# Performance work log

Measured on AMD Instinct MI355X. Metric: run time of the kernel, lower is better.

Reference implementation:

```python
import jax, jax.numpy as jnp
import numpy as np

S, B, DENC, DD, DE, V, T = 49, 64, 512, 1800, 512, 10000, 20


def setup_inputs() -> dict:
    key = jax.random.key(0)
    ks = jax.random.split(key, 16)
    g = lambda i, shape: jax.random.normal(ks[i], shape, jnp.float32) * 0.02
    z = lambda *shape: jnp.zeros(shape, jnp.float32)
    return {
        "h": jax.random.normal(ks[0], (S, B, DENC), jnp.float32),
        "E": jax.random.randint(ks[1], (T, B), 0, V),
        "emb": g(2, (V, DE)),
        "attn_W1": g(3, (DD, DD + DENC)), "attn_b1": z(DD),
        "attn_w2": g(4, (DD,)), "attn_b2": z(),
        "beta_w": g(5, (DD,)), "beta_b": z(),
        "W_ih": g(6, (4 * DD, DE + DENC)), "W_hh": g(7, (4 * DD, DD)),
        "b_ih": z(4 * DD), "b_hh": z(4 * DD),
        "out_W": g(8, (V, DD + DE + DENC)), "out_b": z(V),
        "ih_W1": g(9, (DD, DENC)), "ih_b1": z(DD), "ih_W2": g(10, (DD, DD)), "ih_b2": z(DD),
        "ic_W1": g(11, (DD, DENC)), "ic_b1": z(DD), "ic_W2": g(12, (DD, DD)), "ic_b2": z(DD),
    }


def _mlp(x, W1, b1, W2, b2):
    return jax.nn.relu(x @ W1.T + b1) @ W2.T + b2


def reference(h, E, emb, attn_W1, attn_b1, attn_w2, attn_b2, beta_w, beta_b,
              W_ih, W_hh, b_ih, b_hh, out_W, out_b,
              ih_W1, ih_b1, ih_W2, ih_b2, ic_W1, ic_b1, ic_W2, ic_b2):
    # h: (S, B, DENC) encoder annotations; E: (T, B) teacher tokens.
    h_avg = h.mean(axis=0)                        # (B, DENC)
    h0 = _mlp(h_avg, ih_W1, ih_b1, ih_W2, ih_b2)  # (B, DD)
    c0 = _mlp(h_avg, ic_W1, ic_b1, ic_W2, ic_b2)  # (B, DD)
    tok0 = jnp.zeros((h.shape[1],), jnp.int32)    # first y_tm1 is token 0

    def step(carry, e_t):
        ht, ct, prev_tok = carry
        # --- additive attention (queries=ht, keys=values=h) ---
        qexp = jnp.broadcast_to(ht[None], h.shape[:2] + (ht.shape[-1],))  # (S,B,DD)
        zpre = jnp.concatenate([qexp, h], axis=-1)                        # (S,B,DD+DENC)
        u = jax.nn.relu(zpre @ attn_W1.T + attn_b1) @ attn_w2 + attn_b2   # (S,B)
        a = jax.nn.softmax(u, axis=0)                                     # softmax over seq
        ctx = jnp.einsum('sb,sbe->be', a, h)                              # (B,DENC)
        beta = jax.nn.sigmoid(ht @ beta_w + beta_b)                       # (B,)
        ctx = ctx * beta[:, None]
        # --- LSTM cell on [embed(E_tm1); context] ---
        x = jnp.concatenate([emb[e_t], ctx], axis=-1)                     # (B,DE+DENC)
        gates = x @ W_ih.T + b_ih + ht @ W_hh.T + b_hh                    # (B,4*DD)
        i_g, f_g, g_g, o_g = jnp.split(gates, 4, axis=-1)
        c_new = jax.nn.sigmoid(f_g) * ct + jax.nn.sigmoid(i_g) * jnp.tanh(g_g)
        h_new = jax.nn.sigmoid(o_g) * jnp.tanh(c_new)
        # --- deep output layer: [h_t; embed(argmax prev logits); ctx] ---
        y_emb = emb[prev_tok]
        logits = jnp.concatenate([h_new, y_emb, ctx], axis=-1) @ out_W.T + out_b
        return (h_new, c_new, jnp.argmax(logits, axis=-1).astype(jnp.int32)), logits

    _, logits = jax.lax.scan(step, (h0, c0, tok0), E[:-1])
    return logits  # (T-1, B, V)
```

## Files before the change

### kernel.cpp

```cpp
#include <hip/hip_runtime.h>
#include <hip/hip_bf16.h>
#include <cmath>


namespace {

constexpr int S = 49, B = 64, DENC = 512, DD = 1800, DE = 512, V = 10000, T = 20;
constexpr int KC = DD + DE + DENC;
constexpr int G4 = 4 * DD;
constexpr int KCP = 2848;
constexpr int DDP = 1824;

typedef __attribute__((ext_vector_type(8))) short short8;
typedef __attribute__((ext_vector_type(4))) float f32x4;

__device__ inline float sigf(float x) { return 1.f / (1.f + expf(-x)); }

__device__ inline ushort f2bf_rne(float x) {
  unsigned u = __float_as_uint(x);
  unsigned r = (u + 0x7FFFu + ((u >> 16) & 1u)) >> 16;
  return (ushort)r;
}
__device__ inline void split1(float x, ushort& h, ushort& l) {
  h = f2bf_rne(x);
  float hf = __uint_as_float(((unsigned)h) << 16);
  l = f2bf_rne(x - hf);
}
__device__ inline void split8(float4 a, float4 b, short8& hi, short8& lo) {
  float v[8] = {a.x, a.y, a.z, a.w, b.x, b.y, b.z, b.w};
#pragma unroll
  for (int i = 0; i < 8; ++i) {
    ushort h, l; split1(v[i], h, l);
    hi[i] = (short)h; lo[i] = (short)l;
  }
}
__device__ inline unsigned fkey(float f) {
  unsigned u = __float_as_uint(f);
  return (u & 0x80000000u) ? ~u : (u | 0x80000000u);
}

__global__ __launch_bounds__(256) void hmean_kernel(const float* __restrict__ h,
                                                    float* __restrict__ h_avg) {
  int idx = blockIdx.x * 256 + threadIdx.x;
  if (idx >= B * DENC) return;
  float s = 0.f;
  for (int si = 0; si < S; ++si) s += h[(size_t)si * B * DENC + idx];
  h_avg[idx] = s * (1.0f / (float)S);
}

__global__ __launch_bounds__(256) void mfma_gemm9(
    const ushort* __restrict__ Ahi, const ushort* __restrict__ Alo, int ldap,
    const float* __restrict__ Wa, int ldwa, int Ka,
    const float* __restrict__ Wb, int ldwb, int K,
    float* __restrict__ P, int M, int N, int KP, int kchunk) {
  __shared__ float lds[2][6144];
  const int tid = threadIdx.x;
  const int lane = tid & 63;
  const int wv = tid >> 6;
  const int bn = blockIdx.x * 128;
  const int bm = blockIdx.y * 64;
  const int z = blockIdx.z;
  const int row = lane & 15;
  const int k_begin = z * kchunk;
  const int k_end = min(KP, k_begin + kchunk);

  auto stage = [&](int buf, int k0) {
#pragma unroll
    for (int q = 0; q < 4; ++q) {
      const int u = (wv * 4 + q) * 64 + lane;
      const int lr = u >> 3;
      const int pb = u & 7;
      int col = k0 + (pb ^ (lr & 7)) * 4;
      if (col >= K) col = 0;
      int grow = bn + lr;
      if (grow >= N) grow = N - 1;
      const float* src = (col < Ka) ? (Wa + (size_t)grow * ldwa + col)
                                    : (Wb + (size_t)grow * ldwb + (col - Ka));
      __builtin_amdgcn_global_load_lds(
          (const __attribute__((address_space(1))) unsigned int*)src,
          (__attribute__((address_space(3))) unsigned int*)
              &lds[buf][(wv * 4 + q) * 256 + lane * 4],
          16, 0, 0);
    }
    {
      const int u = wv * 64 + lane;
      const int lr = u >> 2;
      const int pb = u & 3;
      const int col = k0 + (pb ^ (lr & 3)) * 8;
      const ushort* sH = Ahi + (size_t)(bm + lr) * ldap + col;
      const ushort* sL = Alo + (size_t)(bm + lr) * ldap + col;
      __builtin_amdgcn_global_load_lds(
          (const __attribute__((address_space(1))) unsigned int*)sH,
          (__attribute__((address_space(3))) unsigned int*)
              &lds[buf][4096 + u * 4], 16, 0, 0);
      __builtin_amdgcn_global_load_lds(
          (const __attribute__((address_space(1))) unsigned int*)sL,
          (__attribute__((address_space(3))) unsigned int*)
              &lds[buf][5120 + u * 4], 16, 0, 0);
    }
  };

  f32x4 acc[2][4] = {};
  const int nsteps = (k_end > k_begin) ? ((k_end - k_begin) >> 5) : 0;
  if (nsteps) stage(0, k_begin);
  __syncthreads();

  for (int t = 0; t < nsteps; ++t) {
    const int cur = t & 1;
    if (t + 1 < nsteps) stage(cur ^ 1, k_begin + (t + 1) * 32);
    const int c0 = (lane >> 4) * 2;
    float4 w0a, w1a, w0b, w1b;
    {
      const int lrw = wv * 32 + row;
      const float* wb = &lds[cur][lrw * 32];
      w0a = *(const float4*)(wb + ((c0 ^ (lrw & 7)) * 4));
      w1a = *(const float4*)(wb + (((c0 + 1) ^ (lrw & 7)) * 4));
    }
    {
      const int lrw = wv * 32 + 16 + row;
      const float* wb = &lds[cur][lrw * 32];
      w0b = *(const float4*)(wb + ((c0 ^ (lrw & 7)) * 4));
      w1b = *(const float4*)(wb + (((c0 + 1) ^ (lrw & 7)) * 4));
    }
    short8 ah[4], al[4];
#pragma unroll
    for (int ms = 0; ms < 4; ++ms) {
      const int lra = ms * 16 + row;
      const int ca = lane >> 4;
      const int pc = (ca ^ (lra & 3)) * 4;
      ah[ms] = *(const short8*)(&lds[cur][4096 + lra * 16] + pc);
      al[ms] = *(const short8*)(&lds[cur][5120 + lra * 16] + pc);
    }
    short8 wh0, wl0, wh1, wl1;
    split8(w0a, w1a, wh0, wl0);
    split8(w0b, w1b, wh1, wl1);
#pragma unroll
    for (int ms = 0; ms < 4; ++ms) {
      acc[0][ms] = __builtin_amdgcn_mfma_f32_16x16x32_bf16(ah[ms], wh0, acc[0][ms], 0, 0, 0);
      acc[0][ms] = __builtin_amdgcn_mfma_f32_16x16x32_bf16(al[ms], wh0, acc[0][ms], 0, 0, 0);
      acc[0][ms] = __builtin_amdgcn_mfma_f32_16x16x32_bf16(ah[ms], wl0, acc[0][ms], 0, 0, 0);
      acc[1][ms] = __builtin_amdgcn_mfma_f32_16x16x32_bf16(ah[ms], wh1, acc[1][ms], 0, 0, 0);
      acc[1][ms] = __builtin_amdgcn_mfma_f32_16x16x32_bf16(al[ms], wh1, acc[1][ms], 0, 0, 0);
      acc[1][ms] = __builtin_amdgcn_mfma_f32_16x16x32_bf16(ah[ms], wl1, acc[1][ms], 0, 0, 0);
    }
    __syncthreads();
  }

  float* Pz = P + (size_t)z * ((size_t)M * N);
#pragma unroll
  for (int j = 0; j < 2; ++j) {
    const int n = bn + wv * 32 + j * 16 + row;
    if (n >= N) continue;
#pragma unroll
    for (int ms = 0; ms < 4; ++ms) {
      int r0 = bm + ms * 16 + (lane >> 4) * 4;
#pragma unroll
      for (int r = 0; r < 4; ++r)
        Pz[(size_t)(r0 + r) * N + n] = acc[j][ms][r];
    }
  }
}

template <int ACT>
__global__ __launch_bounds__(256) void reduce_k(const float* __restrict__ P, int nz,
                                                int total4, size_t MN, int N,
                                                const float* __restrict__ bias,
                                                float* __restrict__ C) {
  int i4 = blockIdx.x * 256 + threadIdx.x;
  if (i4 >= total4) return;
  size_t idx = (size_t)i4 * 4;
  float4 s = *(const float4*)(P + idx);
  for (int zz = 1; zz < nz; ++zz) {
    float4 t = *(const float4*)(P + (size_t)zz * MN + idx);
    s.x += t.x; s.y += t.y; s.z += t.z; s.w += t.w;
  }
  if (bias) {
    int nn = (int)(idx % (size_t)N);
    s.x += bias[nn]; s.y += bias[nn + 1]; s.z += bias[nn + 2]; s.w += bias[nn + 3];
  }
  if (ACT == 1) {
    s.x = fmaxf(s.x, 0.f); s.y = fmaxf(s.y, 0.f);
    s.z = fmaxf(s.z, 0.f); s.w = fmaxf(s.w, 0.f);
  }
  *(float4*)(C + idx) = s;
}

__global__ __launch_bounds__(256) void reduce_lg(const float* __restrict__ P, int nz,
                                                 const float* __restrict__ bias,
                                                 float* __restrict__ C,
                                                 unsigned long long* __restrict__ amax) {
  const int seg = blockIdx.x, b = blockIdx.y;
  const int tid = threadIdx.x;
  const size_t MN = (size_t)B * V;
  unsigned long long best = 0;
  for (int i = tid; i < 250; i += 256) {
    const int n = seg * 1000 + i * 4;
    const size_t idx = (size_t)b * V + n;
    float4 s = *(const float4*)(P + idx);
    for (int zz = 1; zz < nz; ++zz) {
      float4 t = *(const float4*)(P + (size_t)zz * MN + idx);
      s.x += t.x; s.y += t.y; s.z += t.z; s.w += t.w;
    }
    s.x += bias[n]; s.y += bias[n + 1]; s.z += bias[n + 2]; s.w += bias[n + 3];
    *(float4*)(C + idx) = s;
    float v[4] = {s.x, s.y, s.z, s.w};
#pragma unroll
    for (int j = 0; j < 4; ++j) {
      unsigned long long k =
          ((unsigned long long)fkey(v[j]) << 32) | (unsigned)(~(n + j));
      if (k > best) best = k;
    }
  }
  for (int off = 32; off; off >>= 1) {
    unsigned long long o = __shfl_xor(best, off);
    if (o > best) best = o;
  }
  __shared__ unsigned long long red[4];
  if ((tid & 63) == 0) red[tid >> 6] = best;
  __syncthreads();
  if (tid == 0) {
    for (int w = 1; w < 4; ++w)
      if (red[w] > best) best = red[w];
    atomicMax(&amax[b], best);
  }
}

__global__ __launch_bounds__(256) void split_row(
    const float* __restrict__ Wa, int ldwa, int Ka,
    int KP, ushort* __restrict__ hi, ushort* __restrict__ lo) {
  const int r = blockIdx.x;
  const float* ra = Wa + (size_t)r * ldwa;
  ushort* hr = hi + (size_t)r * KP;
  ushort* lr = lo + (size_t)r * KP;
  for (int k = threadIdx.x * 4; k < KP; k += 1024) {
    float4 v = {0.f, 0.f, 0.f, 0.f};
    if (k + 4 <= Ka) v = *(const float4*)(ra + k);
    ushort h0, l0, h1, l1, h2, l2, h3, l3;
    split1(v.x, h0, l0); split1(v.y, h1, l1);
    split1(v.z, h2, l2); split1(v.w, h3, l3);
    ushort4 hv = {h0, h1, h2, h3}, lv = {l0, l1, l2, l3};
    *(ushort4*)(hr + k) = hv;
    *(ushort4*)(lr + k) = lv;
  }
}

__global__ __launch_bounds__(256) void attn_u_kernel(const float* __restrict__ Q,
                                                     const float* __restrict__ Hproj,
                                                     const float* __restrict__ w2,
                                                     const float* __restrict__ b2,
                                                     float* __restrict__ u) {
  int s = blockIdx.x, b = blockIdx.y;
  const float4* q4 = (const float4*)(Q + (size_t)b * DD);
  const float4* h4 = (const float4*)(Hproj + ((size_t)s * B + b) * DD);
  const float4* w4 = (const float4*)w2;
  float acc = 0.f;
  for (int i = threadIdx.x; i < DD / 4; i += 256) {
    float4 q = q4[i], hh = h4[i], w = w4[i];
    acc += fmaxf(q.x + hh.x, 0.f) * w.x + fmaxf(q.y + hh.y, 0.f) * w.y +
           fmaxf(q.z + hh.z, 0.f) * w.z + fmaxf(q.w + hh.w, 0.f) * w.w;
  }
  for (int off = 32; off; off >>= 1) acc += __shfl_xor(acc, off);
  __shared__ float red[4];
  if ((threadIdx.x & 63) == 0) red[threadIdx.x >> 6] = acc;
  __syncthreads();
  if (threadIdx.x == 0) u[s * B + b] = red[0] + red[1] + red[2] + red[3] + b2[0];
}

__global__ __launch_bounds__(256) void softmax_ctx_pack(
    const float* __restrict__ u, const float* __restrict__ h,
    const float* __restrict__ ht, const float* __restrict__ beta_w,
    const float* __restrict__ beta_b, const float* __restrict__ emb,
    const int* __restrict__ Et, const unsigned long long* __restrict__ amax,
    ushort* __restrict__ xcat_hi, ushort* __restrict__ xcat_lo,
    ushort* __restrict__ cat2_hi, ushort* __restrict__ cat2_lo) {
  int b = blockIdx.x, slice = blockIdx.y, tid = threadIdx.x;
  __shared__ float a_sh[S];
  __shared__ float red[4];
  float uv = (tid < S) ? u[tid * B + b] : -INFINITY;
  float m = uv;
  for (int off = 32; off; off >>= 1) m = fmaxf(m, __shfl_xor(m, off));
  if ((tid & 63) == 0) red[tid >> 6] = m;
  __syncthreads();
  m = fmaxf(fmaxf(red[0], red[1]), fmaxf(red[2], red[3]));
  float e = (tid < S) ? expf(uv - m) : 0.f;
  float ssum = e;
  for (int off = 32; off; off >>= 1) ssum += __shfl_xor(ssum, off);
  __syncthreads();
  if ((tid & 63) == 0) red[tid >> 6] = ssum;
  __syncthreads();
  ssum = red[0] + red[1] + red[2] + red[3];
  if (tid < S) a_sh[tid] = e / ssum;
  float acc = 0.f;
  {
    const float4* h4 = (const float4*)(ht + (size_t)b * DD);
    const float4* w4 = (const float4*)beta_w;
    for (int i = tid; i < DD / 4; i += 256) {
      float4 x = h4[i], w = w4[i];
      acc += x.x * w.x + x.y * w.y + x.z * w.z + x.w * w.w;
    }
  }
  for (int off = 32; off; off >>= 1) acc += __shfl_xor(acc, off);
  __syncthreads();
  if ((tid & 63) == 0) red[tid >> 6] = acc;
  __syncthreads();
  float beta = sigf(red[0] + red[1] + red[2] + red[3] + beta_b[0]);

  const size_t xb = (size_t)b * KCP;
  for (int e0 = slice * 128 + tid; e0 < slice * 128 + 128; e0 += 256) {
    float c = 0.f;
    for (int si = 0; si < S; ++si) c += a_sh[si] * h[((size_t)si * B + b) * DENC + e0];
    c *= beta;
    ushort hh, ll; split1(c, hh, ll);
    xcat_hi[xb + DE + e0] = hh;      xcat_lo[xb + DE + e0] = ll;
    cat2_hi[xb + DD + DE + e0] = hh; cat2_lo[xb + DD + DE + e0] = ll;
  }
  int et = Et[b];
  int pt = (int)(~(unsigned)(amax[b] & 0xFFFFFFFFull));
  for (int e0 = slice * 128 + tid; e0 < slice * 128 + 128; e0 += 256) {
    ushort hh, ll;
    split1(emb[(size_t)et * DE + e0], hh, ll);
    xcat_hi[xb + e0] = hh; xcat_lo[xb + e0] = ll;
    split1(emb[(size_t)pt * DE + e0], hh, ll);
    cat2_hi[xb + DD + e0] = hh; cat2_lo[xb + DD + e0] = ll;
  }
  for (int j = slice * 450 + tid; j < slice * 450 + 450; j += 256) {
    ushort hh, ll; split1(ht[(size_t)b * DD + j], hh, ll);
    xcat_hi[xb + DE + DENC + j] = hh; xcat_lo[xb + DE + DENC + j] = ll;
  }
  if (slice == 3 && tid < KCP - KC) {
    xcat_hi[xb + KC + tid] = 0; xcat_lo[xb + KC + tid] = 0;
    cat2_hi[xb + KC + tid] = 0; cat2_lo[xb + KC + tid] = 0;
  }
}

__global__ __launch_bounds__(256) void lstm_fused(
    const float* __restrict__ P, int nz, const float* __restrict__ b_ih,
    const float* __restrict__ b_hh, float* __restrict__ ct, float* __restrict__ ht,
    ushort* __restrict__ cat2_hi, ushort* __restrict__ cat2_lo,
    ushort* __restrict__ ht_hi, ushort* __restrict__ ht_lo,
    unsigned long long* __restrict__ amax) {
  int idx = blockIdx.x * 256 + threadIdx.x;
  if (idx < B) amax[idx] = 0ull;
  if (idx >= B * DD) return;
  int b = idx / DD, d = idx % DD;
  const size_t MN = (size_t)B * G4;
  float g0 = 0.f, g1 = 0.f, g2 = 0.f, g3 = 0.f;
  for (int zz = 0; zz < nz; ++zz) {
    const float* g = P + (size_t)zz * MN + (size_t)b * G4;
    g0 += g[d]; g1 += g[DD + d]; g2 += g[2 * DD + d]; g3 += g[3 * DD + d];
  }
  g0 += b_ih[d] + b_hh[d];
  g1 += b_ih[DD + d] + b_hh[DD + d];
  g2 += b_ih[2 * DD + d] + b_hh[2 * DD + d];
  g3 += b_ih[3 * DD + d] + b_hh[3 * DD + d];
  float c = sigf(g1) * ct[idx] + sigf(g0) * tanhf(g2);
  float hn = sigf(g3) * tanhf(c);
  ct[idx] = c;
  ht[idx] = hn;
  ushort hh, ll; split1(hn, hh, ll);
  cat2_hi[(size_t)b * KCP + d] = hh; cat2_lo[(size_t)b * KCP + d] = ll;
  ht_hi[(size_t)b * DDP + d] = hh;   ht_lo[(size_t)b * DDP + d] = ll;
  if (d < DDP - DD) {
    ht_hi[(size_t)b * DDP + DD + d] = 0; ht_lo[(size_t)b * DDP + DD + d] = 0;
  }
}

__global__ void init_amax(unsigned long long* amax) {
  if (threadIdx.x < B) amax[threadIdx.x] = 0x00000000FFFFFFFFull;
}

constexpr size_t OFF_HAVG  = 0;
constexpr size_t OFF_TMP   = OFF_HAVG + 32768;
constexpr size_t OFF_HT    = OFF_TMP + 115200;
constexpr size_t OFF_CT    = OFF_HT + 115200;
constexpr size_t OFF_HPROJ = OFF_CT + 115200;
constexpr size_t OFF_Q     = OFF_HPROJ + 5644800;
constexpr size_t OFF_U     = OFF_Q + 115200;
constexpr size_t OFF_TOK   = OFF_U + 3200;
constexpr size_t OFF_PBUF  = OFF_TOK + 128;
constexpr size_t PBUF_F    = 6400000;
constexpr size_t OFF_USH   = OFF_PBUF + PBUF_F;

constexpr size_t U_HT_HI  = 0;
constexpr size_t U_HT_LO  = U_HT_HI + (size_t)B * DDP;
constexpr size_t U_XC_HI  = U_HT_LO + (size_t)B * DDP;
constexpr size_t U_XC_LO  = U_XC_HI + (size_t)B * KCP;
constexpr size_t U_C2_HI  = U_XC_LO + (size_t)B * KCP;
constexpr size_t U_C2_LO  = U_C2_HI + (size_t)B * KCP;
constexpr size_t U_H_HI   = U_C2_LO + (size_t)B * KCP;
constexpr size_t U_H_LO   = U_H_HI + (size_t)(S * B) * DENC;

}

extern "C" void kernel_launch(void* const* d_in, const int* in_sizes, int n_in,
                              void* d_out, int out_size, void* d_ws, size_t ws_size,
                              hipStream_t stream) {
  const float* h       = (const float*)d_in[0];
  const int*   E       = (const int*)d_in[1];
  const float* emb     = (const float*)d_in[2];
  const float* attn_W1 = (const float*)d_in[3];
  const float* attn_b1 = (const float*)d_in[4];
  const float* attn_w2 = (const float*)d_in[5];
  const float* attn_b2 = (const float*)d_in[6];
  const float* beta_w  = (const float*)d_in[7];
  const float* beta_b  = (const float*)d_in[8];
  const float* W_ih    = (const float*)d_in[9];
  const float* W_hh    = (const float*)d_in[10];
  const float* b_ih    = (const float*)d_in[11];
  const float* b_hh    = (const float*)d_in[12];
  const float* out_W   = (const float*)d_in[13];
  const float* out_b   = (const float*)d_in[14];
  const float* ih_W1   = (const float*)d_in[15];
  const float* ih_b1   = (const float*)d_in[16];
  const float* ih_W2   = (const float*)d_in[17];
  const float* ih_b2   = (const float*)d_in[18];
  const float* ic_W1   = (const float*)d_in[19];
  const float* ic_b1   = (const float*)d_in[20];
  const float* ic_W2   = (const float*)d_in[21];
  const float* ic_b2   = (const float*)d_in[22];

  float* ws    = (float*)d_ws;
  float* havg  = ws + OFF_HAVG;
  float* tmp   = ws + OFF_TMP;
  float* ht    = ws + OFF_HT;
  float* ct    = ws + OFF_CT;
  float* Hproj = ws + OFF_HPROJ;
  float* Q     = ws + OFF_Q;
  float* u     = ws + OFF_U;
  unsigned long long* amax = (unsigned long long*)(ws + OFF_TOK);
  float* PBUF  = ws + OFF_PBUF;
  ushort* bfb  = (ushort*)(ws + OFF_USH);
  ushort* ht_hi = bfb + U_HT_HI;
  ushort* ht_lo = bfb + U_HT_LO;
  ushort* xc_hi = bfb + U_XC_HI;
  ushort* xc_lo = bfb + U_XC_LO;
  ushort* c2_hi = bfb + U_C2_HI;
  ushort* c2_lo = bfb + U_C2_LO;
  ushort* h_hi  = bfb + U_H_HI;
  ushort* h_lo  = bfb + U_H_LO;
  float* out   = (float*)d_out;

  ushort* hv_hi = xc_hi;
  ushort* hv_lo = xc_lo;
  ushort* t_hi  = c2_hi;
  ushort* t_lo  = c2_lo;

  auto cdiv = [](int a, int b) { return (a + b - 1) / b; };
  const int BIGK = 1 << 28;

  hmean_kernel<<<cdiv(B * DENC, 256), 256, 0, stream>>>(h, havg);
  split_row<<<B, 256, 0, stream>>>(havg, DENC, DENC, DENC, hv_hi, hv_lo);
  mfma_gemm9<<<dim3(cdiv(DD, 128), 1, 4), 256, 0, stream>>>(
      hv_hi, hv_lo, DENC, ih_W1, DENC, BIGK, ih_W1, DENC, DENC,
      PBUF, B, DD, DENC, 128);
  reduce_k<1><<<cdiv(B * DD / 4, 256), 256, 0, stream>>>(
      PBUF, 4, B * DD / 4, (size_t)B * DD, DD, ih_b1, tmp);
  split_row<<<B, 256, 0, stream>>>(tmp, DD, DD, DDP, t_hi, t_lo);
  mfma_gemm9<<<dim3(cdiv(DD, 128), 1, 12), 256, 0, stream>>>(
      t_hi, t_lo, DDP, ih_W2, DD, BIGK, ih_W2, DD, DD,
      PBUF, B, DD, DDP, 160);
  reduce_k<0><<<cdiv(B * DD / 4, 256), 256, 0, stream>>>(
      PBUF, 12, B * DD / 4, (size_t)B * DD, DD, ih_b2, ht);
  mfma_gemm9<<<dim3(cdiv(DD, 128), 1, 4), 256, 0, stream>>>(
      hv_hi, hv_lo, DENC, ic_W1, DENC, BIGK, ic_W1, DENC, DENC,
      PBUF, B, DD, DENC, 128);
  reduce_k<1><<<cdiv(B * DD / 4, 256), 256, 0, stream>>>(
      PBUF, 4, B * DD / 4, (size_t)B * DD, DD, ic_b1, tmp);
  split_row<<<B, 256, 0, stream>>>(tmp, DD, DD, DDP, t_hi, t_lo);
  mfma_gemm9<<<dim3(cdiv(DD, 128), 1, 12), 256, 0, stream>>>(
      t_hi, t_lo, DDP, ic_W2, DD, BIGK, ic_W2, DD, DD,
      PBUF, B, DD, DDP, 160);
  reduce_k<0><<<cdiv(B * DD / 4, 256), 256, 0, stream>>>(
      PBUF, 12, B * DD / 4, (size_t)B * DD, DD, ic_b2, ct);
  split_row<<<B, 256, 0, stream>>>(ht, DD, DD, DDP, ht_hi, ht_lo);
  split_row<<<S * B, 256, 0, stream>>>(h, DENC, DENC, DENC, h_hi, h_lo);
  mfma_gemm9<<<dim3(cdiv(DD, 128), S * B / 64, 1), 256, 0, stream>>>(
      h_hi, h_lo, DENC, attn_W1 + DD, DD + DENC, BIGK, attn_W1 + DD,
      DD + DENC, DENC, Hproj, S * B, DD, DENC, 512);
  reduce_k<0><<<cdiv(S * B * DD / 4, 256), 256, 0, stream>>>(
      Hproj, 1, S * B * DD / 4, (size_t)S * B * DD, DD, attn_b1, Hproj);
  init_amax<<<1, 64, 0, stream>>>(amax);

  for (int t = 0; t < T - 1; ++t) {
    mfma_gemm9<<<dim3(cdiv(DD, 128), 1, 12), 256, 0, stream>>>(
        ht_hi, ht_lo, DDP, attn_W1, DD + DENC, BIGK, attn_W1, DD + DENC, DD,
        PBUF, B, DD, DDP, 160);
    reduce_k<0><<<cdiv(B * DD / 4, 256), 256, 0, stream>>>(
        PBUF, 12, B * DD / 4, (size_t)B * DD, DD, nullptr, Q);
    attn_u_kernel<<<dim3(S, B), 256, 0, stream>>>(Q, Hproj, attn_w2, attn_b2, u);
    softmax_ctx_pack<<<dim3(B, 4), 256, 0, stream>>>(u, h, ht, beta_w, beta_b, emb,
        E + (size_t)t * B, amax, xc_hi, xc_lo, c2_hi, c2_lo);
    mfma_gemm9<<<dim3(cdiv(G4, 128), 1, 12), 256, 0, stream>>>(
        xc_hi, xc_lo, KCP, W_ih, DE + DENC, DE + DENC, W_hh, DD, KC,
        PBUF, B, G4, KCP, 256);
    lstm_fused<<<cdiv(B * DD, 256), 256, 0, stream>>>(
        PBUF, 12, b_ih, b_hh, ct, ht, c2_hi, c2_lo, ht_hi, ht_lo, amax);
    float* logits_t = out + (size_t)t * B * V;
    mfma_gemm9<<<dim3(cdiv(V, 128), 1, 10), 256, 0, stream>>>(
        c2_hi, c2_lo, KCP, out_W, KC, BIGK, out_W, KC, KC,
        PBUF, B, V, KCP, 288);
    reduce_lg<<<dim3(10, B), 256, 0, stream>>>(PBUF, 10, out_b, logits_t, amax);
  }
  (void)in_sizes; (void)n_in; (void)out_size; (void)ws_size;
}
```

Baseline: 2.088 ms.

## Fuse split-K reduce, attention scores, softmax and context pack into one kernel

Replaces the per-step reduce_k, attn_u_kernel and softmax_ctx_pack launches with a single attn_fused kernel, one block per batch row. The block reduces the split-K partials of the query projection in registers, computes all 49 attention scores and the beta gate, then does softmax, the context sum and the bf16 hi/lo packing. This removes two launches per step and the global round trips for Q and u. In exchange, the grid shrinks to 64 blocks, each streaming all Hproj rows for its batch element, so the device may be underused.

```diff
diff --git a/kernel.cpp b/kernel.cpp
--- a/kernel.cpp
+++ b/kernel.cpp
@@ -244,69 +244,84 @@
   }
 }
 
-__global__ __launch_bounds__(256) void attn_u_kernel(const float* __restrict__ Q,
-                                                     const float* __restrict__ Hproj,
-                                                     const float* __restrict__ w2,
-                                                     const float* __restrict__ b2,
-                                                     float* __restrict__ u) {
-  int s = blockIdx.x, b = blockIdx.y;
-  const float4* q4 = (const float4*)(Q + (size_t)b * DD);
-  const float4* h4 = (const float4*)(Hproj + ((size_t)s * B + b) * DD);
-  const float4* w4 = (const float4*)w2;
-  float acc = 0.f;
-  for (int i = threadIdx.x; i < DD / 4; i += 256) {
-    float4 q = q4[i], hh = h4[i], w = w4[i];
-    acc += fmaxf(q.x + hh.x, 0.f) * w.x + fmaxf(q.y + hh.y, 0.f) * w.y +
-           fmaxf(q.z + hh.z, 0.f) * w.z + fmaxf(q.w + hh.w, 0.f) * w.w;
-  }
-  for (int off = 32; off; off >>= 1) acc += __shfl_xor(acc, off);
-  __shared__ float red[4];
-  if ((threadIdx.x & 63) == 0) red[threadIdx.x >> 6] = acc;
-  __syncthreads();
-  if (threadIdx.x == 0) u[s * B + b] = red[0] + red[1] + red[2] + red[3] + b2[0];
-}
-
-__global__ __launch_bounds__(256) void softmax_ctx_pack(
-    const float* __restrict__ u, const float* __restrict__ h,
-    const float* __restrict__ ht, const float* __restrict__ beta_w,
-    const float* __restrict__ beta_b, const float* __restrict__ emb,
-    const int* __restrict__ Et, const unsigned long long* __restrict__ amax,
+__global__ __launch_bounds__(256) void attn_fused(
+    const float* __restrict__ P, int nz,
+    const float* __restrict__ Hproj,
+    const float* __restrict__ w2, const float* __restrict__ b2,
+    const float* __restrict__ h, const float* __restrict__ ht,
+    const float* __restrict__ beta_w, const float* __restrict__ beta_b,
+    const float* __restrict__ emb, const int* __restrict__ Et,
+    const unsigned long long* __restrict__ amax,
     ushort* __restrict__ xcat_hi, ushort* __restrict__ xcat_lo,
     ushort* __restrict__ cat2_hi, ushort* __restrict__ cat2_lo) {
-  int b = blockIdx.x, slice = blockIdx.y, tid = threadIdx.x;
+  const int b = blockIdx.x, tid = threadIdx.x;
+  const int wv = tid >> 6;
+  __shared__ float redw[S * 4];
+  __shared__ float red_b[4];
+  __shared__ float u_sh[S];
   __shared__ float a_sh[S];
-  __shared__ float red[4];
-  float uv = (tid < S) ? u[tid * B + b] : -INFINITY;
-  float m = uv;
-  for (int off = 32; off; off >>= 1) m = fmaxf(m, __shfl_xor(m, off));
-  if ((tid & 63) == 0) red[tid >> 6] = m;
+
+  const int f0 = tid, f1 = tid + 256;
+  const bool v1 = (f1 < DD / 4);
+
+  float4 q0 = {0.f, 0.f, 0.f, 0.f}, q1 = {0.f, 0.f, 0.f, 0.f};
+  for (int z = 0; z < nz; ++z) {
+    const float* pr = P + (size_t)z * ((size_t)B * DD) + (size_t)b * DD;
+    float4 t0 = *(const float4*)(pr + f0 * 4);
+    q0.x += t0.x; q0.y += t0.y; q0.z += t0.z; q0.w += t0.w;
+    if (v1) {
+      float4 t1 = *(const float4*)(pr + f1 * 4);
+      q1.x += t1.x; q1.y += t1.y; q1.z += t1.z; q1.w += t1.w;
+    }
+  }
+  float4 w0 = *(const float4*)(w2 + f0 * 4);
+  float4 w1 = {0.f, 0.f, 0.f, 0.f};
+  if (v1) w1 = *(const float4*)(w2 + f1 * 4);
+
+  {
+    const float* hr = ht + (size_t)b * DD;
+    float4 x0 = *(const float4*)(hr + f0 * 4);
+    float4 bw0 = *(const float4*)(beta_w + f0 * 4);
+    float p = x0.x * bw0.x + x0.y * bw0.y + x0.z * bw0.z + x0.w * bw0.w;
+    if (v1) {
+      float4 x1 = *(const float4*)(hr + f1 * 4);
+      float4 bw1 = *(const float4*)(beta_w + f1 * 4);
+      p += x1.x * bw1.x + x1.y * bw1.y + x1.z * bw1.z + x1.w * bw1.w;
+    }
+    for (int off = 32; off; off >>= 1) p += __shfl_xor(p, off);
+    if ((tid & 63) == 0) red_b[wv] = p;
+  }
+
+  for (int s = 0; s < S; ++s) {
+    const float* hp = Hproj + ((size_t)s * B + b) * DD;
+    float4 a0 = *(const float4*)(hp + f0 * 4);
+    float p = fmaxf(q0.x + a0.x, 0.f) * w0.x + fmaxf(q0.y + a0.y, 0.f) * w0.y +
+              fmaxf(q0.z + a0.z, 0.f) * w0.z + fmaxf(q0.w + a0.w, 0.f) * w0.w;
+    if (v1) {
+      float4 a1 = *(const float4*)(hp + f1 * 4);
+      p += fmaxf(q1.x + a1.x, 0.f) * w1.x + fmaxf(q1.y + a1.y, 0.f) * w1.y +
+           fmaxf(q1.z + a1.z, 0.f) * w1.z + fmaxf(q1.w + a1.w, 0.f) * w1.w;
+    }
+    for (int off = 32; off; off >>= 1) p += __shfl_xor(p, off);
+    if ((tid & 63) == 0) redw[s * 4 + wv] = p;
+  }
   __syncthreads();
-  m = fmaxf(fmaxf(red[0], red[1]), fmaxf(red[2], red[3]));
-  float e = (tid < S) ? expf(uv - m) : 0.f;
-  float ssum = e;
-  for (int off = 32; off; off >>= 1) ssum += __shfl_xor(ssum, off);
+  float beta = sigf(red_b[0] + red_b[1] + red_b[2] + red_b[3] + beta_b[0]);
+  if (tid < S)
+    u_sh[tid] = redw[tid * 4] + redw[tid * 4 + 1] + redw[tid * 4 + 2] +
+                redw[tid * 4 + 3] + b2[0];
   __syncthreads();
-  if ((tid & 63) == 0) red[tid >> 6] = ssum;
+  if (tid < S) {
+    float m = -INFINITY;
+    for (int s = 0; s < S; ++s) m = fmaxf(m, u_sh[s]);
+    float ssum = 0.f;
+    for (int s = 0; s < S; ++s) ssum += expf(u_sh[s] - m);
+    a_sh[tid] = expf(u_sh[tid] - m) / ssum;
+  }
   __syncthreads();
-  ssum = red[0] + red[1] + red[2] + red[3];
-  if (tid < S) a_sh[tid] = e / ssum;
-  float acc = 0.f;
-  {
-    const float4* h4 = (const float4*)(ht + (size_t)b * DD);
-    const float4* w4 = (const float4*)beta_w;
-    for (int i = tid; i < DD / 4; i += 256) {
-      float4 x = h4[i], w = w4[i];
-      acc += x.x * w.x + x.y * w.y + x.z * w.z + x.w * w.w;
-    }
-  }
-  for (int off = 32; off; off >>= 1) acc += __shfl_xor(acc, off);
-  __syncthreads();
-  if ((tid & 63) == 0) red[tid >> 6] = acc;
-  __syncthreads();
-  float beta = sigf(red[0] + red[1] + red[2] + red[3] + beta_b[0]);
 
   const size_t xb = (size_t)b * KCP;
-  for (int e0 = slice * 128 + tid; e0 < slice * 128 + 128; e0 += 256) {
+  for (int e0 = tid; e0 < DENC; e0 += 256) {
     float c = 0.f;
     for (int si = 0; si < S; ++si) c += a_sh[si] * h[((size_t)si * B + b) * DENC + e0];
     c *= beta;
@@ -316,18 +331,18 @@
   }
   int et = Et[b];
   int pt = (int)(~(unsigned)(amax[b] & 0xFFFFFFFFull));
-  for (int e0 = slice * 128 + tid; e0 < slice * 128 + 128; e0 += 256) {
+  for (int e0 = tid; e0 < DE; e0 += 256) {
     ushort hh, ll;
     split1(emb[(size_t)et * DE + e0], hh, ll);
     xcat_hi[xb + e0] = hh; xcat_lo[xb + e0] = ll;
     split1(emb[(size_t)pt * DE + e0], hh, ll);
     cat2_hi[xb + DD + e0] = hh; cat2_lo[xb + DD + e0] = ll;
   }
-  for (int j = slice * 450 + tid; j < slice * 450 + 450; j += 256) {
+  for (int j = tid; j < DD; j += 256) {
     ushort hh, ll; split1(ht[(size_t)b * DD + j], hh, ll);
     xcat_hi[xb + DE + DENC + j] = hh; xcat_lo[xb + DE + DENC + j] = ll;
   }
-  if (slice == 3 && tid < KCP - KC) {
+  if (tid < KCP - KC) {
     xcat_hi[xb + KC + tid] = 0; xcat_lo[xb + KC + tid] = 0;
     cat2_hi[xb + KC + tid] = 0; cat2_lo[xb + KC + tid] = 0;
   }
@@ -425,8 +440,6 @@
   float* ht    = ws + OFF_HT;
   float* ct    = ws + OFF_CT;
   float* Hproj = ws + OFF_HPROJ;
-  float* Q     = ws + OFF_Q;
-  float* u     = ws + OFF_U;
   unsigned long long* amax = (unsigned long long*)(ws + OFF_TOK);
   float* PBUF  = ws + OFF_PBUF;
   ushort* bfb  = (ushort*)(ws + OFF_USH);
@@ -485,10 +498,8 @@
     mfma_gemm9<<<dim3(cdiv(DD, 128), 1, 12), 256, 0, stream>>>(
         ht_hi, ht_lo, DDP, attn_W1, DD + DENC, BIGK, attn_W1, DD + DENC, DD,
         PBUF, B, DD, DDP, 160);
-    reduce_k<0><<<cdiv(B * DD / 4, 256), 256, 0, stream>>>(
-        PBUF, 12, B * DD / 4, (size_t)B * DD, DD, nullptr, Q);
-    attn_u_kernel<<<dim3(S, B), 256, 0, stream>>>(Q, Hproj, attn_w2, attn_b2, u);
-    softmax_ctx_pack<<<dim3(B, 4), 256, 0, stream>>>(u, h, ht, beta_w, beta_b, emb,
+    attn_fused<<<B, 256, 0, stream>>>(
+        PBUF, 12, Hproj, attn_w2, attn_b2, h, ht, beta_w, beta_b, emb,
         E + (size_t)t * B, amax, xc_hi, xc_lo, c2_hi, c2_lo);
     mfma_gemm9<<<dim3(cdiv(G4, 128), 1, 12), 256, 0, stream>>>(
         xc_hi, xc_lo, KCP, W_ih, DE + DENC, DE + DENC, W_hh, DD, KC,
```

Result: slower. 2.801 ms (+34.2%).
